# Optimization experiments

Hardware: AMD Instinct MI355X
Metric: run time of the kernel (lower is better)

The kernel has to match this reference:

```python
import jax, jax.numpy as jnp
import numpy as np

N_NODES = 100000
N_EDGES = 640000
HIDDEN = 128
EPS = 1e-6


def setup_inputs() -> dict:
    key = jax.random.key(0)
    k_x, k_w, k_a, k_e = jax.random.split(key, 4)
    x = jax.random.normal(k_x, (N_NODES, HIDDEN), dtype=jnp.float32)
    W = jax.random.normal(k_w, (HIDDEN, HIDDEN), dtype=jnp.float32) / np.sqrt(HIDDEN)
    b = jnp.zeros((HIDDEN,), dtype=jnp.float32)
    att_w = jax.random.normal(k_a, (1, 2 * HIDDEN), dtype=jnp.float32) / np.sqrt(2 * HIDDEN)
    norm_w = jnp.ones((HIDDEN,), dtype=jnp.float32)
    norm_b = jnp.zeros((HIDDEN,), dtype=jnp.float32)
    e = jax.random.randint(k_e, (N_EDGES, 2), 0, N_NODES, dtype=jnp.int64)
    return {"x": x, "W": W, "b": b, "att_w": att_w, "norm_w": norm_w, "norm_b": norm_b, "e": e}


def reference(x, W, b, att_w, norm_w, norm_b, e):
    n_nodes = x.shape[0]
    src, dst = e[:, 0], e[:, 1]
    # Edge gather + shared linear on both endpoints: [E, D]
    m = x[src] @ W.T + b
    s = x[dst] @ W.T + b
    # Attention score per edge: leaky_relu(concat @ w^T), then exp -> [E, 1]
    a = jnp.exp(jax.nn.leaky_relu(jnp.concatenate((m, s), axis=1) @ att_w.T, negative_slope=0.2))
    # NOTE: faithful to the original: this weighted message sum is computed
    # but then overwritten (dead code in the source module).
    _unused = jax.ops.segment_sum(a * m, dst, num_segments=n_nodes)
    # Normalizer: sum of attention weights per destination node -> [N, 1]
    n = jax.ops.segment_sum(a, dst, num_segments=n_nodes)
    h = jax.nn.relu(x / jnp.where(n == 0.0, 1.0, n))
    # Residual + RMSNorm (per-row, with affine weight and bias, eps=1e-6)
    y = h + x
    inv_rms = jax.lax.rsqrt(jnp.mean(y * y, axis=-1, keepdims=True) + EPS)
    return norm_w * (y * inv_rms) + norm_b
```

## Files before the change

kernel.cpp:

```cpp
#include <hip/hip_runtime.h>

#define N_NODES 100000
#define N_EDGES 640000
#define HIDDEN  128
#define EPS     1e-6f

__global__ void precompute_uvc(const float* __restrict__ W,
                               const float* __restrict__ b,
                               const float* __restrict__ att_w,
                               float* __restrict__ u,
                               float* __restrict__ v,
                               float* __restrict__ c) {
    __shared__ float su_s[4][HIDDEN];
    __shared__ float sv_s[4][HIDDEN];
    int k     = threadIdx.x & 127;
    int chunk = threadIdx.x >> 7;

    float su = 0.f, sv = 0.f;
    #pragma unroll
    for (int jj = 0; jj < 32; ++jj) {
        int j = chunk * 32 + jj;
        float w = W[j * HIDDEN + k];
        su += att_w[j] * w;
        sv += att_w[HIDDEN + j] * w;
    }
    su_s[chunk][k] = su;
    sv_s[chunk][k] = sv;

    if (threadIdx.x < 64) {
        int t0 = threadIdx.x, t1 = threadIdx.x + 64;
        float t = att_w[t0] * b[t0] + att_w[HIDDEN + t0] * b[t0]
                + att_w[t1] * b[t1] + att_w[HIDDEN + t1] * b[t1];
        #pragma unroll
        for (int off = 32; off > 0; off >>= 1) t += __shfl_xor(t, off);
        if (threadIdx.x == 0) *c = t;
    }

    __syncthreads();
    if (chunk == 0) {
        u[k] = su_s[0][k] + su_s[1][k] + su_s[2][k] + su_s[3][k];
        v[k] = sv_s[0][k] + sv_s[1][k] + sv_s[2][k] + sv_s[3][k];
    }
}

__global__ void node_dots(const float* __restrict__ x,
                          const float* __restrict__ u,
                          const float* __restrict__ v,
                          float* __restrict__ p,
                          float* __restrict__ q,
                          float* __restrict__ nacc) {
    int gid  = blockIdx.x * blockDim.x + threadIdx.x;
    int wave = gid >> 6;
    int lane = threadIdx.x & 63;
    int half = lane >> 5;
    int sub  = lane & 31;
    int node = wave * 2 + half;
    if (node >= N_NODES) return;

    float4 xv = ((const float4*)(x + (size_t)node * HIDDEN))[sub];
    float4 uv = ((const float4*)u)[sub];
    float4 vv = ((const float4*)v)[sub];

    float sp = xv.x * uv.x + xv.y * uv.y + xv.z * uv.z + xv.w * uv.w;
    float sq = xv.x * vv.x + xv.y * vv.y + xv.z * vv.z + xv.w * vv.w;
    #pragma unroll
    for (int off = 16; off > 0; off >>= 1) {
        sp += __shfl_xor(sp, off);
        sq += __shfl_xor(sq, off);
    }
    if (sub == 0) {
        p[node]    = sp;
        q[node]    = sq;
        nacc[node] = 0.f;
    }
}

__global__ void edge_kernel(const int* __restrict__ e,
                            const float* __restrict__ p,
                            const float* __restrict__ q,
                            const float* __restrict__ c,
                            float* __restrict__ nacc) {
    int eid = blockIdx.x * blockDim.x + threadIdx.x;
    if (eid >= N_EDGES) return;
    int2 ed = ((const int2*)e)[eid];
    float score = p[ed.x] + q[ed.y] + c[0];
    float lr = score > 0.f ? score : 0.2f * score;
    atomicAdd(&nacc[ed.y], __expf(lr) == __expf(lr) ? expf(lr) : expf(lr));
}

__global__ void final_kernel(const float* __restrict__ x,
                             const float* __restrict__ nacc,
                             const float* __restrict__ norm_w,
                             const float* __restrict__ norm_b,
                             float* __restrict__ out) {
    int gid  = blockIdx.x * blockDim.x + threadIdx.x;
    int wave = gid >> 6;
    int lane = threadIdx.x & 63;
    int half = lane >> 5;
    int sub  = lane & 31;
    int node = wave * 2 + half;
    if (node >= N_NODES) return;

    float nn = nacc[node];
    float inv_n = 1.f / (nn == 0.f ? 1.f : nn);

    float4 xv = ((const float4*)(x + (size_t)node * HIDDEN))[sub];
    float4 y;
    {
        float h;
        h = xv.x * inv_n; h = h > 0.f ? h : 0.f; y.x = h + xv.x;
        h = xv.y * inv_n; h = h > 0.f ? h : 0.f; y.y = h + xv.y;
        h = xv.z * inv_n; h = h > 0.f ? h : 0.f; y.z = h + xv.z;
        h = xv.w * inv_n; h = h > 0.f ? h : 0.f; y.w = h + xv.w;
    }

    float ss = y.x * y.x + y.y * y.y + y.z * y.z + y.w * y.w;
    #pragma unroll
    for (int off = 16; off > 0; off >>= 1) ss += __shfl_xor(ss, off);
    float inv_rms = rsqrtf(ss * (1.f / HIDDEN) + EPS);

    float4 wv = ((const float4*)norm_w)[sub];
    float4 bv = ((const float4*)norm_b)[sub];
    float4 ov;
    ov.x = wv.x * (y.x * inv_rms) + bv.x;
    ov.y = wv.y * (y.y * inv_rms) + bv.y;
    ov.z = wv.z * (y.z * inv_rms) + bv.z;
    ov.w = wv.w * (y.w * inv_rms) + bv.w;
    ((float4*)(out + (size_t)node * HIDDEN))[sub] = ov;
}

extern "C" void kernel_launch(void* const* d_in, const int* in_sizes, int n_in,
                              void* d_out, int out_size, void* d_ws, size_t ws_size,
                              hipStream_t stream) {
    const float* x      = (const float*)d_in[0];
    const float* W      = (const float*)d_in[1];
    const float* b      = (const float*)d_in[2];
    const float* att_w  = (const float*)d_in[3];
    const float* norm_w = (const float*)d_in[4];
    const float* norm_b = (const float*)d_in[5];
    const int*   e      = (const int*)d_in[6];
    float* out = (float*)d_out;

    float* ws = (float*)d_ws;
    float* u    = ws;
    float* v    = ws + 128;
    float* c    = ws + 256;
    float* p    = ws + 1024;
    float* q    = p + N_NODES;
    float* nacc = q + N_NODES;

    precompute_uvc<<<1, 512, 0, stream>>>(W, b, att_w, u, v, c);

    {
        int blocks = (N_NODES + 7) / 8;
        node_dots<<<blocks, 256, 0, stream>>>(x, u, v, p, q, nacc);
    }
    {
        int blocks = (N_EDGES + 255) / 256;
        edge_kernel<<<blocks, 256, 0, stream>>>(e, p, q, c, nacc);
    }
    {
        int blocks = (N_NODES + 7) / 8;
        final_kernel<<<blocks, 256, 0, stream>>>(x, nacc, norm_w, norm_b, out);
    }
}
```

Before: 160.2 us.

## Fuse all four GAT stages into one cooperative persistent kernel

Replaces the four separate launches (u/v/c precompute, node dots, edge scatter, final RMSNorm) with a single cooperative kernel that uses grid-wide syncs between phases. Each block recomputes u, v and c redundantly in shared memory instead of reading them from a separate launch. The goal is to remove launch overhead and inter-kernel gaps. In exchange it adds the cost of grid.sync, repeats the W reduction in every block, and caps parallelism at a persistent grid of at most 1024 blocks.

After: 359.5 us. 124% more time.

```diff
diff --git a/kernel.cpp b/kernel.cpp
--- a/kernel.cpp
+++ b/kernel.cpp
@@ -1,132 +1,131 @@
 #include <hip/hip_runtime.h>
+#include <hip/hip_cooperative_groups.h>
+
+namespace cg = cooperative_groups;
 
 #define N_NODES 100000
 #define N_EDGES 640000
 #define HIDDEN  128
 #define EPS     1e-6f
+#define NUM_CU  256
 
-__global__ void precompute_uvc(const float* __restrict__ W,
-                               const float* __restrict__ b,
-                               const float* __restrict__ att_w,
-                               float* __restrict__ u,
-                               float* __restrict__ v,
-                               float* __restrict__ c) {
-    __shared__ float su_s[4][HIDDEN];
-    __shared__ float sv_s[4][HIDDEN];
-    int k     = threadIdx.x & 127;
-    int chunk = threadIdx.x >> 7;
+__global__ __launch_bounds__(256, 4)
+void fused_gat(const float* __restrict__ x,
+               const float* __restrict__ W,
+               const float* __restrict__ b,
+               const float* __restrict__ att_w,
+               const float* __restrict__ norm_w,
+               const float* __restrict__ norm_b,
+               const int*   __restrict__ e,
+               float* __restrict__ out,
+               float* __restrict__ p,
+               float* __restrict__ q,
+               float* __restrict__ nacc) {
+    __shared__ float su_s[2][HIDDEN];
+    __shared__ float sv_s[2][HIDDEN];
+    __shared__ float u_s[HIDDEN];
+    __shared__ float v_s[HIDDEN];
+    __shared__ float c_s;
 
-    float su = 0.f, sv = 0.f;
-    #pragma unroll
-    for (int jj = 0; jj < 32; ++jj) {
-        int j = chunk * 32 + jj;
-        float w = W[j * HIDDEN + k];
-        su += att_w[j] * w;
-        sv += att_w[HIDDEN + j] * w;
+    const int tid = threadIdx.x;
+    const int k = tid & 127;
+    const int h128 = tid >> 7;
+
+    {
+        float su = 0.f, sv = 0.f;
+        #pragma unroll 8
+        for (int jj = 0; jj < 64; ++jj) {
+            int j = h128 * 64 + jj;
+            float w = W[j * HIDDEN + k];
+            su += att_w[j] * w;
+            sv += att_w[HIDDEN + j] * w;
+        }
+        su_s[h128][k] = su;
+        sv_s[h128][k] = sv;
     }
-    su_s[chunk][k] = su;
-    sv_s[chunk][k] = sv;
-
-    if (threadIdx.x < 64) {
-        int t0 = threadIdx.x, t1 = threadIdx.x + 64;
-        float t = att_w[t0] * b[t0] + att_w[HIDDEN + t0] * b[t0]
-                + att_w[t1] * b[t1] + att_w[HIDDEN + t1] * b[t1];
+    __syncthreads();
+    if (tid < 128) {
+        u_s[k] = su_s[0][k] + su_s[1][k];
+        v_s[k] = sv_s[0][k] + sv_s[1][k];
+    } else if (tid < 192) {
+        int l = tid - 128;
+        float t = att_w[l] * b[l] + att_w[HIDDEN + l] * b[l]
+                + att_w[l + 64] * b[l + 64] + att_w[HIDDEN + l + 64] * b[l + 64];
         #pragma unroll
         for (int off = 32; off > 0; off >>= 1) t += __shfl_xor(t, off);
-        if (threadIdx.x == 0) *c = t;
+        if (l == 0) c_s = t;
+    }
+    __syncthreads();
+
+    cg::grid_group grid = cg::this_grid();
+
+    const int gwave  = (int)((blockIdx.x * blockDim.x + tid) >> 6);
+    const int nwaves = (int)((gridDim.x * blockDim.x) >> 6);
+    const int lane   = tid & 63;
+    const int halfw  = lane >> 5;
+    const int sub    = lane & 31;
+
+    const float4 uv = ((const float4*)u_s)[sub];
+    const float4 vv = ((const float4*)v_s)[sub];
+
+    for (int node = gwave * 2 + halfw; node < N_NODES; node += nwaves * 2) {
+        float4 xv = ((const float4*)(x + (size_t)node * HIDDEN))[sub];
+        float sp = xv.x * uv.x + xv.y * uv.y + xv.z * uv.z + xv.w * uv.w;
+        float sq = xv.x * vv.x + xv.y * vv.y + xv.z * vv.z + xv.w * vv.w;
+        #pragma unroll
+        for (int off = 16; off > 0; off >>= 1) {
+            sp += __shfl_xor(sp, off);
+            sq += __shfl_xor(sq, off);
+        }
+        if (sub == 0) {
+            p[node] = sp;
+            q[node] = sq;
+            nacc[node] = 0.f;
+        }
     }
 
-    __syncthreads();
-    if (chunk == 0) {
-        u[k] = su_s[0][k] + su_s[1][k] + su_s[2][k] + su_s[3][k];
-        v[k] = sv_s[0][k] + sv_s[1][k] + sv_s[2][k] + sv_s[3][k];
-    }
-}
+    grid.sync();
 
-__global__ void node_dots(const float* __restrict__ x,
-                          const float* __restrict__ u,
-                          const float* __restrict__ v,
-                          float* __restrict__ p,
-                          float* __restrict__ q,
-                          float* __restrict__ nacc) {
-    int gid  = blockIdx.x * blockDim.x + threadIdx.x;
-    int wave = gid >> 6;
-    int lane = threadIdx.x & 63;
-    int half = lane >> 5;
-    int sub  = lane & 31;
-    int node = wave * 2 + half;
-    if (node >= N_NODES) return;
-
-    float4 xv = ((const float4*)(x + (size_t)node * HIDDEN))[sub];
-    float4 uv = ((const float4*)u)[sub];
-    float4 vv = ((const float4*)v)[sub];
-
-    float sp = xv.x * uv.x + xv.y * uv.y + xv.z * uv.z + xv.w * uv.w;
-    float sq = xv.x * vv.x + xv.y * vv.y + xv.z * vv.z + xv.w * vv.w;
-    #pragma unroll
-    for (int off = 16; off > 0; off >>= 1) {
-        sp += __shfl_xor(sp, off);
-        sq += __shfl_xor(sq, off);
-    }
-    if (sub == 0) {
-        p[node]    = sp;
-        q[node]    = sq;
-        nacc[node] = 0.f;
-    }
-}
-
-__global__ void edge_kernel(const int* __restrict__ e,
-                            const float* __restrict__ p,
-                            const float* __restrict__ q,
-                            const float* __restrict__ c,
-                            float* __restrict__ nacc) {
-    int eid = blockIdx.x * blockDim.x + threadIdx.x;
-    if (eid >= N_EDGES) return;
-    int2 ed = ((const int2*)e)[eid];
-    float score = p[ed.x] + q[ed.y] + c[0];
-    float lr = score > 0.f ? score : 0.2f * score;
-    atomicAdd(&nacc[ed.y], __expf(lr) == __expf(lr) ? expf(lr) : expf(lr));
-}
-
-__global__ void final_kernel(const float* __restrict__ x,
-                             const float* __restrict__ nacc,
-                             const float* __restrict__ norm_w,
-                             const float* __restrict__ norm_b,
-                             float* __restrict__ out) {
-    int gid  = blockIdx.x * blockDim.x + threadIdx.x;
-    int wave = gid >> 6;
-    int lane = threadIdx.x & 63;
-    int half = lane >> 5;
-    int sub  = lane & 31;
-    int node = wave * 2 + half;
-    if (node >= N_NODES) return;
-
-    float nn = nacc[node];
-    float inv_n = 1.f / (nn == 0.f ? 1.f : nn);
-
-    float4 xv = ((const float4*)(x + (size_t)node * HIDDEN))[sub];
-    float4 y;
     {
-        float h;
-        h = xv.x * inv_n; h = h > 0.f ? h : 0.f; y.x = h + xv.x;
-        h = xv.y * inv_n; h = h > 0.f ? h : 0.f; y.y = h + xv.y;
-        h = xv.z * inv_n; h = h > 0.f ? h : 0.f; y.z = h + xv.z;
-        h = xv.w * inv_n; h = h > 0.f ? h : 0.f; y.w = h + xv.w;
+        const float c = c_s;
+        const int nthreads = (int)(gridDim.x * blockDim.x);
+        for (int eid = (int)(blockIdx.x * blockDim.x) + tid; eid < N_EDGES; eid += nthreads) {
+            int2 ed = ((const int2*)e)[eid];
+            float score = p[ed.x] + q[ed.y] + c;
+            float lr = score > 0.f ? score : 0.2f * score;
+            atomicAdd(&nacc[ed.y], expf(lr));
+        }
     }
 
-    float ss = y.x * y.x + y.y * y.y + y.z * y.z + y.w * y.w;
-    #pragma unroll
-    for (int off = 16; off > 0; off >>= 1) ss += __shfl_xor(ss, off);
-    float inv_rms = rsqrtf(ss * (1.f / HIDDEN) + EPS);
+    grid.sync();
 
-    float4 wv = ((const float4*)norm_w)[sub];
-    float4 bv = ((const float4*)norm_b)[sub];
-    float4 ov;
-    ov.x = wv.x * (y.x * inv_rms) + bv.x;
-    ov.y = wv.y * (y.y * inv_rms) + bv.y;
-    ov.z = wv.z * (y.z * inv_rms) + bv.z;
-    ov.w = wv.w * (y.w * inv_rms) + bv.w;
-    ((float4*)(out + (size_t)node * HIDDEN))[sub] = ov;
+    {
+        const float4 wv = ((const float4*)norm_w)[sub];
+        const float4 bv = ((const float4*)norm_b)[sub];
+        for (int node = gwave * 2 + halfw; node < N_NODES; node += nwaves * 2) {
+            float nn = nacc[node];
+            float inv_n = 1.f / (nn == 0.f ? 1.f : nn);
+            float4 xv = ((const float4*)(x + (size_t)node * HIDDEN))[sub];
+            float4 y;
+            float h;
+            h = xv.x * inv_n; h = h > 0.f ? h : 0.f; y.x = h + xv.x;
+            h = xv.y * inv_n; h = h > 0.f ? h : 0.f; y.y = h + xv.y;
+            h = xv.z * inv_n; h = h > 0.f ? h : 0.f; y.z = h + xv.z;
+            h = xv.w * inv_n; h = h > 0.f ? h : 0.f; y.w = h + xv.w;
+
+            float ss = y.x * y.x + y.y * y.y + y.z * y.z + y.w * y.w;
+            #pragma unroll
+            for (int off = 16; off > 0; off >>= 1) ss += __shfl_xor(ss, off);
+            float inv_rms = rsqrtf(ss * (1.f / HIDDEN) + EPS);
+
+            float4 ov;
+            ov.x = wv.x * (y.x * inv_rms) + bv.x;
+            ov.y = wv.y * (y.y * inv_rms) + bv.y;
+            ov.z = wv.z * (y.z * inv_rms) + bv.z;
+            ov.w = wv.w * (y.w * inv_rms) + bv.w;
+            ((float4*)(out + (size_t)node * HIDDEN))[sub] = ov;
+        }
+    }
 }
 
 extern "C" void kernel_launch(void* const* d_in, const int* in_sizes, int n_in,
@@ -141,26 +140,24 @@
     const int*   e      = (const int*)d_in[6];
     float* out = (float*)d_out;
 
-    float* ws = (float*)d_ws;
-    float* u    = ws;
-    float* v    = ws + 128;
-    float* c    = ws + 256;
-    float* p    = ws + 1024;
+    float* ws   = (float*)d_ws;
+    float* p    = ws;
     float* q    = p + N_NODES;
     float* nacc = q + N_NODES;
 
-    precompute_uvc<<<1, 512, 0, stream>>>(W, b, att_w, u, v, c);
+    int maxBlocksPerCU = 0;
+    hipOccupancyMaxActiveBlocksPerMultiprocessor(&maxBlocksPerCU,
+                                                 (const void*)fused_gat, 256, 0);
+    if (maxBlocksPerCU < 1) maxBlocksPerCU = 1;
+    int nblocks = maxBlocksPerCU * NUM_CU;
+    if (nblocks > 1024) nblocks = 1024;
 
-    {
-        int blocks = (N_NODES + 7) / 8;
-        node_dots<<<blocks, 256, 0, stream>>>(x, u, v, p, q, nacc);
-    }
-    {
-        int blocks = (N_EDGES + 255) / 256;
-        edge_kernel<<<blocks, 256, 0, stream>>>(e, p, q, c, nacc);
-    }
-    {
-        int blocks = (N_NODES + 7) / 8;
-        final_kernel<<<blocks, 256, 0, stream>>>(x, nacc, norm_w, norm_b, out);
-    }
+    void* args[] = {
+        (void*)&x, (void*)&W, (void*)&b, (void*)&att_w,
+        (void*)&norm_w, (void*)&norm_b, (void*)&e,
+        (void*)&out, (void*)&p, (void*)&q, (void*)&nacc
+    };
+    hipLaunchCooperativeKernel((const void*)fused_gat,
+                               dim3(nblocks), dim3(256),
+                               args, 0, stream);
 }
```
